# Kernel optimization log

Hardware: AMD Instinct MI355X
Metric: run time of the kernel (lower is better)

## Reference

```python
import jax, jax.numpy as jnp
import numpy as np

DMODEL = 1024
NHEADS = 16
FFN = 4 * DMODEL
HEAD_DIM = DMODEL // NHEADS
SCALE = HEAD_DIM ** -0.5


def layer_norm(x, gamma, beta, eps=1e-5):
    mu = jnp.mean(x, axis=-1, keepdims=True)
    var = jnp.var(x, axis=-1, keepdims=True)
    return (x - mu) * jax.lax.rsqrt(var + eps) * gamma + beta


def setup_inputs() -> dict:
    key = jax.random.key(0)
    ks = jax.random.split(key, 8)
    std = 0.02
    B, S = 2, 2048
    return {
        "src": jax.random.normal(ks[0], (B, S, DMODEL), jnp.float32),
        "pre_gamma": jnp.ones((DMODEL,), jnp.float32),
        "pre_beta": jnp.zeros((DMODEL,), jnp.float32),
        "qkv_w": jax.random.truncated_normal(ks[1], -2.0, 2.0, (3 * DMODEL, DMODEL), jnp.float32) * std,
        "qkv_b": jnp.zeros((3 * DMODEL,), jnp.float32),
        "addnorm_gamma": jnp.ones((DMODEL,), jnp.float32),
        "addnorm_beta": jnp.zeros((DMODEL,), jnp.float32),
        "fc1_w": jax.random.truncated_normal(ks[2], -2.0, 2.0, (FFN, DMODEL), jnp.float32) * std,
        "fc1_b": jnp.zeros((FFN,), jnp.float32),
        "fc2_w": jax.random.truncated_normal(ks[3], -2.0, 2.0, (DMODEL, FFN), jnp.float32) * std,
        "fc2_b": jnp.zeros((DMODEL,), jnp.float32),
    }


def reference(src, pre_gamma, pre_beta, qkv_w, qkv_b, addnorm_gamma, addnorm_beta,
              fc1_w, fc1_b, fc2_w, fc2_b):
    B, S, D = src.shape
    # PreNorm
    x = layer_norm(src, pre_gamma, pre_beta)
    # MHSA (no output projection, matching source)
    qkv = x @ qkv_w.T + qkv_b  # [B,S,3D]
    q, k, v = jnp.split(qkv, 3, axis=-1)
    def heads(t):
        return t.reshape(B, S, NHEADS, HEAD_DIM).transpose(0, 2, 1, 3)  # [B,H,S,hd]
    q, k, v = heads(q), heads(k), heads(v)
    attn = jnp.einsum("bhqd,bhkd->bhqk", q, k) * SCALE
    attn = jax.nn.softmax(attn, axis=-1)
    attn_out = jnp.einsum("bhqk,bhkd->bhqd", attn, v)
    attn_out = attn_out.transpose(0, 2, 1, 3).reshape(B, S, D)
    # shared AddNorm #1
    x = layer_norm(attn_out + x, addnorm_gamma, addnorm_beta)
    # FFN
    h = jax.nn.gelu(x @ fc1_w.T + fc1_b, approximate=False)
    ffn_out = h @ fc2_w.T + fc2_b
    # shared AddNorm #2 (same params as #1)
    return layer_norm(ffn_out + x, addnorm_gamma, addnorm_beta)
```

## Files before the change

### kernel.cpp

```cpp
#include <hip/hip_runtime.h>
#include <hip/hip_bf16.h>
#include <math.h>

#define DMODEL 1024
#define NH 16
#define HD 64
#define SEQ 2048
#define BATCH 2
#define MROWS (BATCH * SEQ)
#define FFN_DIM 4096

using bf16x8 = __attribute__((ext_vector_type(8))) __bf16;
using f32x4  = __attribute__((ext_vector_type(4))) float;

typedef const __attribute__((address_space(1))) unsigned char* gas_t;
typedef __attribute__((address_space(3))) unsigned char* las_t;

__device__ inline unsigned short f2bf(float f) {
    unsigned int u = __builtin_bit_cast(unsigned int, f);
    u += 0x7fffu + ((u >> 16) & 1u);
    return (unsigned short)(u >> 16);
}
__device__ inline unsigned short f2bf_up(float f) {
    unsigned int u = __builtin_bit_cast(unsigned int, f);
    return (unsigned short)((u + 0x8000u) >> 16);
}
__device__ inline float bf2f(unsigned short u) {
    unsigned int v = ((unsigned int)u) << 16;
    return __builtin_bit_cast(float, v);
}
__device__ inline float gelu_f(float x) {
    float x2 = x * x;
    float w = x * fmaf(0.07135481627f, x2, 1.59576912161f);
    return x / (1.0f + __expf(-w));
}

__global__ __launch_bounds__(256) void ln_pre_cvt(
        const float* __restrict__ a,
        const float* __restrict__ gamma, const float* __restrict__ beta,
        float* __restrict__ out_f, unsigned short* __restrict__ out_b,
        const float* __restrict__ wa, unsigned short* __restrict__ oa, int na4,
        const float* __restrict__ wb, unsigned short* __restrict__ ob, int nb4,
        const float* __restrict__ wc, unsigned char* __restrict__ oc, int nc4) {
    int blk = blockIdx.x;
    int t = threadIdx.x;
    if (blk >= MROWS) {
        int i = (blk - MROWS) * 256 + t;
        if (i < na4) {
            float4 v = ((const float4*)wa)[i];
            ushort4 o;
            o.x = f2bf(v.x); o.y = f2bf(v.y); o.z = f2bf(v.z); o.w = f2bf(v.w);
            ((ushort4*)oa)[i] = o;
        } else if (i < na4 + nb4) {
            int j = i - na4;
            float4 v = ((const float4*)wb)[j];
            ushort4 o;
            o.x = f2bf(v.x); o.y = f2bf(v.y); o.z = f2bf(v.z); o.w = f2bf(v.w);
            ((ushort4*)ob)[j] = o;
        } else if (i < na4 + nb4 + nc4) {
            int j = i - na4 - nb4;
            float4 v = ((const float4*)wc)[j];
            int pk = __builtin_amdgcn_cvt_pk_fp8_f32(v.x, v.y, 0, false);
            pk     = __builtin_amdgcn_cvt_pk_fp8_f32(v.z, v.w, pk, true);
            ((unsigned int*)oc)[j] = (unsigned int)pk;
        }
        return;
    }
    int row = blk;
    float4 v = ((const float4*)(a + (size_t)row * DMODEL))[t];
    float s  = v.x + v.y + v.z + v.w;
    float s2 = v.x * v.x + v.y * v.y + v.z * v.z + v.w * v.w;
    #pragma unroll
    for (int off = 32; off > 0; off >>= 1) {
        s  += __shfl_xor(s,  off, 64);
        s2 += __shfl_xor(s2, off, 64);
    }
    __shared__ float red[8];
    int wave = t >> 6, lane = t & 63;
    if (lane == 0) { red[wave] = s; red[4 + wave] = s2; }
    __syncthreads();
    float tot  = red[0] + red[1] + red[2] + red[3];
    float tot2 = red[4] + red[5] + red[6] + red[7];
    float mu   = tot * (1.0f / DMODEL);
    float var  = tot2 * (1.0f / DMODEL) - mu * mu;
    float rstd = rsqrtf(var + 1e-5f);
    float4 g  = ((const float4*)gamma)[t];
    float4 be = ((const float4*)beta)[t];
    float4 o;
    o.x = (v.x - mu) * rstd * g.x + be.x;
    o.y = (v.y - mu) * rstd * g.y + be.y;
    o.z = (v.z - mu) * rstd * g.z + be.z;
    o.w = (v.w - mu) * rstd * g.w + be.w;
    ((float4*)(out_f + (size_t)row * DMODEL))[t] = o;
    ushort4 ob4;
    ob4.x = f2bf(o.x); ob4.y = f2bf(o.y); ob4.z = f2bf(o.z); ob4.w = f2bf(o.w);
    ((ushort4*)(out_b + (size_t)row * DMODEL))[t] = ob4;
}

__global__ __launch_bounds__(256) void ln_attn(
        const float* __restrict__ o0, const float* __restrict__ o1,
        const float* __restrict__ l0, const float* __restrict__ l1,
        const float* __restrict__ xres,
        const float* __restrict__ gamma, const float* __restrict__ beta,
        float* __restrict__ out_f, unsigned short* __restrict__ out_b) {
    int row = blockIdx.x;
    int t = threadIdx.x;
    int b_ = row >> 11, s = row & 2047;
    int h = t >> 4;
    int bh = b_ * NH + h;
    size_t obase = ((size_t)bh * SEQ + s) * HD + (4 * t & 63);
    float4 va = ((const float4*)(o0 + obase))[0];
    float4 vb = ((const float4*)(o1 + obase))[0];
    float inv_l = 1.0f / (l0[(size_t)bh * SEQ + s] + l1[(size_t)bh * SEQ + s]);
    float4 rr = ((const float4*)(xres + (size_t)row * DMODEL))[t];
    float4 v;
    v.x = (va.x + vb.x) * inv_l + rr.x;
    v.y = (va.y + vb.y) * inv_l + rr.y;
    v.z = (va.z + vb.z) * inv_l + rr.z;
    v.w = (va.w + vb.w) * inv_l + rr.w;

    float s1 = v.x + v.y + v.z + v.w;
    float s2 = v.x * v.x + v.y * v.y + v.z * v.z + v.w * v.w;
    #pragma unroll
    for (int off = 32; off > 0; off >>= 1) {
        s1 += __shfl_xor(s1, off, 64);
        s2 += __shfl_xor(s2, off, 64);
    }
    __shared__ float red[8];
    int wave = t >> 6, lane = t & 63;
    if (lane == 0) { red[wave] = s1; red[4 + wave] = s2; }
    __syncthreads();
    float tot  = red[0] + red[1] + red[2] + red[3];
    float tot2 = red[4] + red[5] + red[6] + red[7];
    float mu   = tot * (1.0f / DMODEL);
    float var  = tot2 * (1.0f / DMODEL) - mu * mu;
    float rstd = rsqrtf(var + 1e-5f);
    float4 g  = ((const float4*)gamma)[t];
    float4 be = ((const float4*)beta)[t];
    float4 o;
    o.x = (v.x - mu) * rstd * g.x + be.x;
    o.y = (v.y - mu) * rstd * g.y + be.y;
    o.z = (v.z - mu) * rstd * g.z + be.z;
    o.w = (v.w - mu) * rstd * g.w + be.w;
    ((float4*)(out_f + (size_t)row * DMODEL))[t] = o;
    ushort4 ob;
    ob.x = f2bf(o.x); ob.y = f2bf(o.y); ob.z = f2bf(o.z); ob.w = f2bf(o.w);
    ((ushort4*)(out_b + (size_t)row * DMODEL))[t] = ob;
}

__global__ __launch_bounds__(256) void ln_fc2(
        const unsigned short* __restrict__ p0, const unsigned short* __restrict__ p1,
        const unsigned short* __restrict__ p2, const unsigned short* __restrict__ p3,
        const float* __restrict__ bias, const float* __restrict__ resid,
        const float* __restrict__ gamma, const float* __restrict__ beta,
        float* __restrict__ out_f) {
    int row = blockIdx.x;
    int t = threadIdx.x;
    size_t base = (size_t)row * DMODEL;
    ushort4 u0 = ((const ushort4*)(p0 + base))[t];
    ushort4 u1 = ((const ushort4*)(p1 + base))[t];
    ushort4 u2 = ((const ushort4*)(p2 + base))[t];
    ushort4 u3 = ((const ushort4*)(p3 + base))[t];
    float4 bb = ((const float4*)bias)[t];
    float4 rr = ((const float4*)(resid + base))[t];
    float4 v;
    v.x = bf2f(u0.x) + bf2f(u1.x) + bf2f(u2.x) + bf2f(u3.x) + bb.x + rr.x;
    v.y = bf2f(u0.y) + bf2f(u1.y) + bf2f(u2.y) + bf2f(u3.y) + bb.y + rr.y;
    v.z = bf2f(u0.z) + bf2f(u1.z) + bf2f(u2.z) + bf2f(u3.z) + bb.z + rr.z;
    v.w = bf2f(u0.w) + bf2f(u1.w) + bf2f(u2.w) + bf2f(u3.w) + bb.w + rr.w;

    float s  = v.x + v.y + v.z + v.w;
    float s2 = v.x * v.x + v.y * v.y + v.z * v.z + v.w * v.w;
    #pragma unroll
    for (int off = 32; off > 0; off >>= 1) {
        s  += __shfl_xor(s,  off, 64);
        s2 += __shfl_xor(s2, off, 64);
    }
    __shared__ float red[8];
    int wave = t >> 6, lane = t & 63;
    if (lane == 0) { red[wave] = s; red[4 + wave] = s2; }
    __syncthreads();
    float tot  = red[0] + red[1] + red[2] + red[3];
    float tot2 = red[4] + red[5] + red[6] + red[7];
    float mu   = tot * (1.0f / DMODEL);
    float var  = tot2 * (1.0f / DMODEL) - mu * mu;
    float rstd = rsqrtf(var + 1e-5f);
    float4 g  = ((const float4*)gamma)[t];
    float4 be = ((const float4*)beta)[t];
    float4 o;
    o.x = (v.x - mu) * rstd * g.x + be.x;
    o.y = (v.y - mu) * rstd * g.y + be.y;
    o.z = (v.z - mu) * rstd * g.z + be.z;
    o.w = (v.w - mu) * rstd * g.w + be.w;
    ((float4*)(out_f + base))[t] = o;
}

template <int MODE>
__global__ __launch_bounds__(256) void gemm_lds(
        const unsigned short* __restrict__ A,
        const unsigned short* __restrict__ Bw,
        const float* __restrict__ bias,
        void* __restrict__ out, int M, int N, int K) {
    __shared__ unsigned short As[128 * 64];
    __shared__ unsigned short Bs[128 * 64];

    const int tid  = threadIdx.x;
    const int wave = tid >> 6;
    const int lane = tid & 63;
    const int quad = lane >> 4;
    const int cc   = lane & 15;
    const int bn = blockIdx.x * 128;
    const int bm = blockIdx.y * 128;

    const unsigned short* Ab = A  + (size_t)bm * K;
    const unsigned short* Bb = Bw + (size_t)bn * K;

    const int srow0 = tid >> 3;
    const int sslot = tid & 7;
    const int rsw   = (cc >> 1) & 7;
    const int wm = (wave >> 1) * 64;
    const int wn = (wave & 1) * 64;

    f32x4 acc[4][4] = {};

    for (int k0 = 0; k0 < K; k0 += 64) {
        #pragma unroll
        for (int i = 0; i < 4; ++i) {
            int row = i * 32 + srow0;
            int g   = sslot ^ ((row >> 1) & 7);
            const unsigned short* ga = Ab + (size_t)row * K + k0 + g * 8;
            const unsigned short* gb = Bb + (size_t)row * K + k0 + g * 8;
            unsigned short* la = &As[i * 2048 + wave * 512];
            unsigned short* lb = &Bs[i * 2048 + wave * 512];
            __builtin_amdgcn_global_load_lds((gas_t)(const void*)ga, (las_t)(void*)la, 16, 0, 0);
            __builtin_amdgcn_global_load_lds((gas_t)(const void*)gb, (las_t)(void*)lb, 16, 0, 0);
        }
        __syncthreads();

        bf16x8 af[4][2], bf[4][2];
        #pragma unroll
        for (int mt = 0; mt < 4; ++mt)
            #pragma unroll
            for (int s = 0; s < 2; ++s) {
                int slot = (s * 4 + quad) ^ rsw;
                af[mt][s] = *(const bf16x8*)&As[(wm + mt * 16 + cc) * 64 + slot * 8];
            }
        #pragma unroll
        for (int nt = 0; nt < 4; ++nt)
            #pragma unroll
            for (int s = 0; s < 2; ++s) {
                int slot = (s * 4 + quad) ^ rsw;
                bf[nt][s] = *(const bf16x8*)&Bs[(wn + nt * 16 + cc) * 64 + slot * 8];
            }

        #pragma unroll
        for (int mt = 0; mt < 4; ++mt)
            #pragma unroll
            for (int nt = 0; nt < 4; ++nt) {
                acc[mt][nt] = __builtin_amdgcn_mfma_f32_16x16x32_bf16(
                    af[mt][0], bf[nt][0], acc[mt][nt], 0, 0, 0);
                acc[mt][nt] = __builtin_amdgcn_mfma_f32_16x16x32_bf16(
                    af[mt][1], bf[nt][1], acc[mt][nt], 0, 0, 0);
            }

        __syncthreads();
    }

    #pragma unroll
    for (int mt = 0; mt < 4; ++mt)
        #pragma unroll
        for (int nt = 0; nt < 4; ++nt) {
            if constexpr (MODE == 1) {
                int m0 = bm + wm + mt * 16 + quad * 4;
                int n  = bn + wn + nt * 16 + cc;
                float bn_ = bias[n];
                float v0 = gelu_f(acc[mt][nt][0] + bn_);
                float v1 = gelu_f(acc[mt][nt][1] + bn_);
                float v2 = gelu_f(acc[mt][nt][2] + bn_);
                float v3 = gelu_f(acc[mt][nt][3] + bn_);
                int pk = __builtin_amdgcn_cvt_pk_fp8_f32(v0, v1, 0, false);
                pk     = __builtin_amdgcn_cvt_pk_fp8_f32(v2, v3, pk, true);
                unsigned char* o = (unsigned char*)out + (size_t)m0 * N + n;
                o[0]             = (unsigned char)pk;
                o[(size_t)N]     = (unsigned char)(pk >> 8);
                o[(size_t)2 * N] = (unsigned char)(pk >> 16);
                o[(size_t)3 * N] = (unsigned char)(pk >> 24);
            } else {
                #pragma unroll
                for (int r = 0; r < 4; ++r) {
                    int m = bm + wm + mt * 16 + quad * 4 + r;
                    int n = bn + wn + nt * 16 + cc;
                    float v = acc[mt][nt][r] + bias[n];
                    int b_ = m >> 11, srow = m & 2047;
                    int which = n >> 10, rem = n & 1023;
                    int h = rem >> 6, d = rem & 63;
                    if (which == 0) v *= 0.125f;
                    size_t idx = ((((size_t)which * BATCH + b_) * NH + h) * SEQ + srow) * HD + d;
                    ((unsigned short*)out)[idx] = f2bf(v);
                }
            }
        }
}

__global__ __launch_bounds__(256) void gemm_fp8(
        const unsigned char* __restrict__ A,
        const unsigned char* __restrict__ Bw,
        unsigned short* __restrict__ p0, unsigned short* __restrict__ p1,
        unsigned short* __restrict__ p2, unsigned short* __restrict__ p3,
        int M, int N, int K, int KC) {
    __shared__ unsigned char As[128 * 64];
    __shared__ unsigned char Bs[128 * 64];

    const int tid  = threadIdx.x;
    const int wave = tid >> 6;
    const int lane = tid & 63;
    const int quad = lane >> 4;
    const int cc   = lane & 15;
    const int bn = blockIdx.x * 128;
    const int bm = blockIdx.y * 128;

    const unsigned char* Ab = A  + (size_t)bm * K;
    const unsigned char* Bb = Bw + (size_t)bn * K;

    const int srow0 = tid >> 2;
    const int schunk = tid & 3;
    const int rsw = (cc >> 1) & 3;
    const int wm = (wave >> 1) * 64;
    const int wn = (wave & 1) * 64;

    const int kbeg = blockIdx.z * KC;
    const int kend = kbeg + KC;

    f32x4 acc[4][4] = {};

    for (int k0 = kbeg; k0 < kend; k0 += 64) {
        #pragma unroll
        for (int i = 0; i < 2; ++i) {
            int row = i * 64 + srow0;
            int g   = schunk ^ ((row >> 1) & 3);
            const unsigned char* ga = Ab + (size_t)row * K + k0 + g * 16;
            const unsigned char* gb = Bb + (size_t)row * K + k0 + g * 16;
            unsigned char* la = &As[i * 4096 + wave * 1024];
            unsigned char* lb = &Bs[i * 4096 + wave * 1024];
            __builtin_amdgcn_global_load_lds((gas_t)(const void*)ga, (las_t)(void*)la, 16, 0, 0);
            __builtin_amdgcn_global_load_lds((gas_t)(const void*)gb, (las_t)(void*)lb, 16, 0, 0);
        }
        __syncthreads();

        long af[4][2], bf[4][2];
        #pragma unroll
        for (int mt = 0; mt < 4; ++mt)
            #pragma unroll
            for (int s = 0; s < 2; ++s) {
                int slot = ((quad >> 1) + 2 * s) ^ rsw;
                af[mt][s] = *(const long*)&As[(wm + mt * 16 + cc) * 64 + slot * 16 + (quad & 1) * 8];
            }
        #pragma unroll
        for (int nt = 0; nt < 4; ++nt)
            #pragma unroll
            for (int s = 0; s < 2; ++s) {
                int slot = ((quad >> 1) + 2 * s) ^ rsw;
                bf[nt][s] = *(const long*)&Bs[(wn + nt * 16 + cc) * 64 + slot * 16 + (quad & 1) * 8];
            }

        #pragma unroll
        for (int mt = 0; mt < 4; ++mt)
            #pragma unroll
            for (int nt = 0; nt < 4; ++nt) {
                acc[mt][nt] = __builtin_amdgcn_mfma_f32_16x16x32_fp8_fp8(
                    af[mt][0], bf[nt][0], acc[mt][nt], 0, 0, 0);
                acc[mt][nt] = __builtin_amdgcn_mfma_f32_16x16x32_fp8_fp8(
                    af[mt][1], bf[nt][1], acc[mt][nt], 0, 0, 0);
            }

        __syncthreads();
    }

    unsigned short* outp = (blockIdx.z == 0) ? p0
                         : (blockIdx.z == 1) ? p1
                         : (blockIdx.z == 2) ? p2 : p3;
    #pragma unroll
    for (int mt = 0; mt < 4; ++mt)
        #pragma unroll
        for (int nt = 0; nt < 4; ++nt)
            #pragma unroll
            for (int r = 0; r < 4; ++r) {
                int m = bm + wm + mt * 16 + quad * 4 + r;
                int n = bn + wn + nt * 16 + cc;
                outp[(size_t)m * N + n] = f2bf(acc[mt][nt][r]);
            }
}

__global__ __launch_bounds__(256) void transpose_v(
        const unsigned short* __restrict__ vsrc, unsigned short* __restrict__ vt) {
    __shared__ unsigned short Ls[64 * 72];
    const int t = threadIdx.x;
    const int s0 = blockIdx.x * 64;
    const int bh = blockIdx.y;
    const unsigned short* in = vsrc + (size_t)bh * SEQ * HD;
    unsigned short* outp = vt + (size_t)bh * SEQ * HD;

    const int row = t >> 2;
    const int c8  = (t & 3) * 8;
    #pragma unroll
    for (int p = 0; p < 2; ++p)
        *(uint4*)&Ls[row * 72 + c8 + p * 32] =
            *(const uint4*)&in[(size_t)(s0 + row) * HD + c8 + p * 32];
    __syncthreads();

    const int hd = t >> 2;
    #pragma unroll
    for (int p = 0; p < 2; ++p) {
        unsigned short tmp[8];
        #pragma unroll
        for (int j = 0; j < 8; ++j)
            tmp[j] = Ls[(c8 + p * 32 + j) * 72 + hd];
        *(uint4*)&outp[(size_t)hd * SEQ + s0 + c8 + p * 32] = *(uint4*)tmp;
    }
}

#define KPAD 72
__global__ __launch_bounds__(256, 4) void attn_mfma(
        const unsigned short* __restrict__ qkv,
        const unsigned short* __restrict__ vt,
        float* __restrict__ op0, float* __restrict__ op1,
        float* __restrict__ lpart) {
    const int tid  = threadIdx.x;
    const int wave = tid >> 6;
    const int lane = tid & 63;
    const int quad = lane >> 4;
    const int cc   = lane & 15;
    const int qblk = blockIdx.x;
    const int bh   = blockIdx.y;
    const int half = blockIdx.z;

    const size_t headsz = (size_t)SEQ * HD;
    const unsigned short* qb  = qkv + (size_t)bh * headsz;
    const unsigned short* kb  = qkv + ((size_t)BATCH * NH + bh) * headsz;
    const unsigned short* vtb = vt + (size_t)bh * headsz;
    float* opart = half ? op1 : op0;
    float* lp    = lpart + (size_t)half * BATCH * NH * SEQ;

    __shared__ unsigned short Ks[64 * KPAD];
    __shared__ unsigned short Vt[64 * KPAD];
    __shared__ unsigned short Ps[4 * 32 * KPAD];

    bf16x8 qa[2][2];
    #pragma unroll
    for (int mt = 0; mt < 2; ++mt) {
        const unsigned short* qp =
            qb + (size_t)(qblk * 128 + wave * 32 + mt * 16 + cc) * HD + quad * 8;
        qa[mt][0] = *(const bf16x8*)qp;
        qa[mt][1] = *(const bf16x8*)(qp + 32);
    }

    f32x4 o_acc[2][4] = {};
    float l_i[2][4] = {};

    const int srow = wave * 16 + (lane >> 2);
    const int sc8  = (lane & 3) * 8;
    const int psw  = (cc >> 2) & 3;

    for (int kt = half * 16; kt < half * 16 + 16; ++kt) {
        __syncthreads();
        #pragma unroll
        for (int p = 0; p < 2; ++p) {
            int col = sc8 + p * 32;
            *(uint4*)&Ks[srow * KPAD + col] =
                *(const uint4*)&kb[(size_t)(kt * 64 + srow) * HD + col];
            *(uint4*)&Vt[srow * KPAD + col] =
                *(const uint4*)&vtb[(size_t)srow * SEQ + kt * 64 + col];
        }
        __syncthreads();

        f32x4 s_acc[2][4];
        #pragma unroll
        for (int nt = 0; nt < 4; ++nt) {
            const unsigned short* kp = &Ks[(nt * 16 + cc) * KPAD + quad * 8];
            bf16x8 kf0 = *(const bf16x8*)kp;
            bf16x8 kf1 = *(const bf16x8*)(kp + 32);
            #pragma unroll
            for (int mt = 0; mt < 2; ++mt) {
                f32x4 z = {};
                z = __builtin_amdgcn_mfma_f32_16x16x32_bf16(qa[mt][0], kf0, z, 0, 0, 0);
                s_acc[mt][nt] = __builtin_amdgcn_mfma_f32_16x16x32_bf16(qa[mt][1], kf1, z, 0, 0, 0);
            }
        }

        unsigned short* pw = &Ps[wave * 32 * KPAD];
        #pragma unroll
        for (int mt = 0; mt < 2; ++mt)
            #pragma unroll
            for (int nt = 0; nt < 4; ++nt) {
                int pc = ((nt ^ quad) & 3) * 16 + cc;
                #pragma unroll
                for (int r = 0; r < 4; ++r) {
                    float e = __expf(s_acc[mt][nt][r]);
                    l_i[mt][r] += e;
                    pw[(mt * 16 + quad * 4 + r) * KPAD + pc] = f2bf_up(e);
                }
            }

        bf16x8 pf[2][2];
        #pragma unroll
        for (int mt = 0; mt < 2; ++mt) {
            const unsigned short* pa = &pw[(mt * 16 + cc) * KPAD];
            pf[mt][0] = *(const bf16x8*)&pa[((((quad >> 1))     ^ psw) & 3) * 16 + (quad & 1) * 8];
            pf[mt][1] = *(const bf16x8*)&pa[(((2 + (quad >> 1)) ^ psw) & 3) * 16 + (quad & 1) * 8];
        }

        #pragma unroll
        for (int nt = 0; nt < 4; ++nt) {
            const unsigned short* vp = &Vt[(nt * 16 + cc) * KPAD + quad * 8];
            bf16x8 vf0 = *(const bf16x8*)vp;
            bf16x8 vf1 = *(const bf16x8*)(vp + 32);
            #pragma unroll
            for (int mt = 0; mt < 2; ++mt) {
                o_acc[mt][nt] = __builtin_amdgcn_mfma_f32_16x16x32_bf16(
                    pf[mt][0], vf0, o_acc[mt][nt], 0, 0, 0);
                o_acc[mt][nt] = __builtin_amdgcn_mfma_f32_16x16x32_bf16(
                    pf[mt][1], vf1, o_acc[mt][nt], 0, 0, 0);
            }
        }
    }

    #pragma unroll
    for (int mt = 0; mt < 2; ++mt) {
        float lr[4];
        #pragma unroll
        for (int r = 0; r < 4; ++r) {
            float l = l_i[mt][r];
            #pragma unroll
            for (int off = 1; off < 16; off <<= 1)
                l += __shfl_xor(l, off, 64);
            lr[r] = l;
        }
        int rowbase = qblk * 128 + wave * 32 + mt * 16;
        if (cc == 0) {
            float4 lv = {lr[0], lr[1], lr[2], lr[3]};
            *(float4*)&lp[(size_t)bh * SEQ + rowbase + quad * 4] = lv;
        }
        #pragma unroll
        for (int nt = 0; nt < 4; ++nt)
            #pragma unroll
            for (int r = 0; r < 4; ++r) {
                int row = rowbase + quad * 4 + r;
                opart[((size_t)bh * SEQ + row) * HD + nt * 16 + cc] = o_acc[mt][nt][r];
            }
    }
}

extern "C" void kernel_launch(void* const* d_in, const int* in_sizes, int n_in,
                              void* d_out, int out_size, void* d_ws, size_t ws_size,
                              hipStream_t stream) {
    const float* src       = (const float*)d_in[0];
    const float* pre_gamma = (const float*)d_in[1];
    const float* pre_beta  = (const float*)d_in[2];
    const float* qkv_w     = (const float*)d_in[3];
    const float* qkv_b     = (const float*)d_in[4];
    const float* an_gamma  = (const float*)d_in[5];
    const float* an_beta   = (const float*)d_in[6];
    const float* fc1_w     = (const float*)d_in[7];
    const float* fc1_b     = (const float*)d_in[8];
    const float* fc2_w     = (const float*)d_in[9];
    const float* fc2_b     = (const float*)d_in[10];
    float* out = (float*)d_out;

    char* ws = (char*)d_ws;
    size_t off = 0;
    auto alloc = [&](size_t bytes) {
        char* p = ws + off;
        off += (bytes + 255) & ~(size_t)255;
        return p;
    };
    float*          x_f   = (float*)alloc((size_t)MROWS * DMODEL * 4);
    unsigned short* x_b   = (unsigned short*)alloc((size_t)MROWS * DMODEL * 2);
    float*          y_f   = (float*)alloc((size_t)MROWS * DMODEL * 4);
    unsigned short* y_b   = (unsigned short*)alloc((size_t)MROWS * DMODEL * 2);
    float*          atf   = (float*)alloc((size_t)MROWS * DMODEL * 4);
    float*          fff   = (float*)alloc((size_t)MROWS * DMODEL * 4);
    unsigned short* qkvb  = (unsigned short*)alloc((size_t)3 * MROWS * DMODEL * 2);
    unsigned char*  h8    = (unsigned char*)alloc((size_t)MROWS * FFN_DIM * 2);
    unsigned short* wqkv  = (unsigned short*)alloc((size_t)3 * DMODEL * DMODEL * 2);
    unsigned short* wfc1  = (unsigned short*)alloc((size_t)FFN_DIM * DMODEL * 2);
    unsigned char*  wfc28 = (unsigned char*)alloc((size_t)DMODEL * FFN_DIM);

    unsigned short* vt_b = (unsigned short*)fff;
    float* opart0 = atf;
    float* opart1 = (float*)h8;
    float* lpart  = (float*)x_b;
    unsigned short* fc2p0 = (unsigned short*)fff;
    unsigned short* fc2p1 = (unsigned short*)x_f;
    unsigned short* fc2p2 = (unsigned short*)atf;
    unsigned short* fc2p3 = (unsigned short*)qkvb;

    int n_qkv4 = 3 * DMODEL * DMODEL / 4;
    int n_fc4  = FFN_DIM * DMODEL / 4;
    int cvt_blocks = (n_qkv4 + 2 * n_fc4 + 255) / 256;

    ln_pre_cvt<<<dim3(MROWS + cvt_blocks), dim3(256), 0, stream>>>(
        src, pre_gamma, pre_beta, x_f, x_b,
        qkv_w, wqkv, n_qkv4, fc1_w, wfc1, n_fc4, fc2_w, wfc28, n_fc4);

    gemm_lds<3><<<dim3(3 * DMODEL / 128, MROWS / 128), dim3(256), 0, stream>>>(
        x_b, wqkv, qkv_b, qkvb, MROWS, 3 * DMODEL, DMODEL);
    transpose_v<<<dim3(SEQ / 64, BATCH * NH), dim3(256), 0, stream>>>(
        qkvb + (size_t)2 * BATCH * NH * SEQ * HD, vt_b);
    attn_mfma<<<dim3(SEQ / 128, BATCH * NH, 2), dim3(256), 0, stream>>>(
        qkvb, vt_b, opart0, opart1, lpart);
    ln_attn<<<dim3(MROWS), dim3(256), 0, stream>>>(
        opart0, opart1, lpart, lpart + (size_t)BATCH * NH * SEQ,
        x_f, an_gamma, an_beta, y_f, y_b);
    gemm_lds<1><<<dim3(FFN_DIM / 128, MROWS / 128), dim3(256), 0, stream>>>(
        y_b, wfc1, fc1_b, h8, MROWS, FFN_DIM, DMODEL);
    gemm_fp8<<<dim3(DMODEL / 128, MROWS / 128, 4), dim3(256), 0, stream>>>(
        h8, wfc28, fc2p0, fc2p1, fc2p2, fc2p3, MROWS, DMODEL, FFN_DIM, 1024);
    ln_fc2<<<dim3(MROWS), dim3(256), 0, stream>>>(
        fc2p0, fc2p1, fc2p2, fc2p3, fc2_b, y_f, an_gamma, an_beta, out);
}
```

Before: 336.5 us.

## Double-buffer LDS tiles in bf16 and fp8 GEMM kernels

Both GEMM kernels now keep two LDS buffers and issue global-to-LDS loads for the next K tile before computing on the current one. The per-iteration barrier count drops from two to one, and memory latency can overlap with MFMA work. In exchange, LDS use per block doubles, which may reduce occupancy. The single barrier after compute relies on how global_load_lds completion interacts with s_waitcnt at __syncthreads.

```diff
diff --git a/kernel.cpp b/kernel.cpp
--- a/kernel.cpp
+++ b/kernel.cpp
@@ -201,8 +201,8 @@
         const unsigned short* __restrict__ Bw,
         const float* __restrict__ bias,
         void* __restrict__ out, int M, int N, int K) {
-    __shared__ unsigned short As[128 * 64];
-    __shared__ unsigned short Bs[128 * 64];
+    __shared__ unsigned short As[2][128 * 64];
+    __shared__ unsigned short Bs[2][128 * 64];
 
     const int tid  = threadIdx.x;
     const int wave = tid >> 6;
@@ -223,19 +223,27 @@
 
     f32x4 acc[4][4] = {};
 
-    for (int k0 = 0; k0 < K; k0 += 64) {
+    auto stage = [&](int buf, int k0) {
         #pragma unroll
         for (int i = 0; i < 4; ++i) {
             int row = i * 32 + srow0;
             int g   = sslot ^ ((row >> 1) & 7);
             const unsigned short* ga = Ab + (size_t)row * K + k0 + g * 8;
             const unsigned short* gb = Bb + (size_t)row * K + k0 + g * 8;
-            unsigned short* la = &As[i * 2048 + wave * 512];
-            unsigned short* lb = &Bs[i * 2048 + wave * 512];
+            unsigned short* la = &As[buf][i * 2048 + wave * 512];
+            unsigned short* lb = &Bs[buf][i * 2048 + wave * 512];
             __builtin_amdgcn_global_load_lds((gas_t)(const void*)ga, (las_t)(void*)la, 16, 0, 0);
             __builtin_amdgcn_global_load_lds((gas_t)(const void*)gb, (las_t)(void*)lb, 16, 0, 0);
         }
-        __syncthreads();
+    };
+
+    const int nkt = K >> 6;
+    stage(0, 0);
+    __syncthreads();
+
+    int cur = 0;
+    for (int kt = 0; kt < nkt; ++kt) {
+        if (kt + 1 < nkt) stage(cur ^ 1, (kt + 1) << 6);
 
         bf16x8 af[4][2], bf[4][2];
         #pragma unroll
@@ -243,14 +251,14 @@
             #pragma unroll
             for (int s = 0; s < 2; ++s) {
                 int slot = (s * 4 + quad) ^ rsw;
-                af[mt][s] = *(const bf16x8*)&As[(wm + mt * 16 + cc) * 64 + slot * 8];
+                af[mt][s] = *(const bf16x8*)&As[cur][(wm + mt * 16 + cc) * 64 + slot * 8];
             }
         #pragma unroll
         for (int nt = 0; nt < 4; ++nt)
             #pragma unroll
             for (int s = 0; s < 2; ++s) {
                 int slot = (s * 4 + quad) ^ rsw;
-                bf[nt][s] = *(const bf16x8*)&Bs[(wn + nt * 16 + cc) * 64 + slot * 8];
+                bf[nt][s] = *(const bf16x8*)&Bs[cur][(wn + nt * 16 + cc) * 64 + slot * 8];
             }
 
         #pragma unroll
@@ -263,7 +271,8 @@
                     af[mt][1], bf[nt][1], acc[mt][nt], 0, 0, 0);
             }
 
-        __syncthreads();
+        if (kt + 1 < nkt) __syncthreads();
+        cur ^= 1;
     }
 
     #pragma unroll
@@ -308,8 +317,8 @@
         unsigned short* __restrict__ p0, unsigned short* __restrict__ p1,
         unsigned short* __restrict__ p2, unsigned short* __restrict__ p3,
         int M, int N, int K, int KC) {
-    __shared__ unsigned char As[128 * 64];
-    __shared__ unsigned char Bs[128 * 64];
+    __shared__ unsigned char As[2][128 * 64];
+    __shared__ unsigned char Bs[2][128 * 64];
 
     const int tid  = threadIdx.x;
     const int wave = tid >> 6;
@@ -329,23 +338,30 @@
     const int wn = (wave & 1) * 64;
 
     const int kbeg = blockIdx.z * KC;
-    const int kend = kbeg + KC;
 
     f32x4 acc[4][4] = {};
 
-    for (int k0 = kbeg; k0 < kend; k0 += 64) {
+    auto stage = [&](int buf, int k0) {
         #pragma unroll
         for (int i = 0; i < 2; ++i) {
             int row = i * 64 + srow0;
             int g   = schunk ^ ((row >> 1) & 3);
             const unsigned char* ga = Ab + (size_t)row * K + k0 + g * 16;
             const unsigned char* gb = Bb + (size_t)row * K + k0 + g * 16;
-            unsigned char* la = &As[i * 4096 + wave * 1024];
-            unsigned char* lb = &Bs[i * 4096 + wave * 1024];
+            unsigned char* la = &As[buf][i * 4096 + wave * 1024];
+            unsigned char* lb = &Bs[buf][i * 4096 + wave * 1024];
             __builtin_amdgcn_global_load_lds((gas_t)(const void*)ga, (las_t)(void*)la, 16, 0, 0);
             __builtin_amdgcn_global_load_lds((gas_t)(const void*)gb, (las_t)(void*)lb, 16, 0, 0);
         }
-        __syncthreads();
+    };
+
+    const int nkt = KC >> 6;
+    stage(0, kbeg);
+    __syncthreads();
+
+    int cur = 0;
+    for (int kt = 0; kt < nkt; ++kt) {
+        if (kt + 1 < nkt) stage(cur ^ 1, kbeg + ((kt + 1) << 6));
 
         long af[4][2], bf[4][2];
         #pragma unroll
@@ -353,14 +369,14 @@
             #pragma unroll
             for (int s = 0; s < 2; ++s) {
                 int slot = ((quad >> 1) + 2 * s) ^ rsw;
-                af[mt][s] = *(const long*)&As[(wm + mt * 16 + cc) * 64 + slot * 16 + (quad & 1) * 8];
+                af[mt][s] = *(const long*)&As[cur][(wm + mt * 16 + cc) * 64 + slot * 16 + (quad & 1) * 8];
             }
         #pragma unroll
         for (int nt = 0; nt < 4; ++nt)
             #pragma unroll
             for (int s = 0; s < 2; ++s) {
                 int slot = ((quad >> 1) + 2 * s) ^ rsw;
-                bf[nt][s] = *(const long*)&Bs[(wn + nt * 16 + cc) * 64 + slot * 16 + (quad & 1) * 8];
+                bf[nt][s] = *(const long*)&Bs[cur][(wn + nt * 16 + cc) * 64 + slot * 16 + (quad & 1) * 8];
             }
 
         #pragma unroll
@@ -373,7 +389,8 @@
                     af[mt][1], bf[nt][1], acc[mt][nt], 0, 0, 0);
             }
 
-        __syncthreads();
+        if (kt + 1 < nkt) __syncthreads();
+        cur ^= 1;
     }
 
     unsigned short* outp = (blockIdx.z == 0) ? p0
```

Result: faster. 323.6 us (-3.8%).
